# Kernel tuning notes

Hardware: AMD Instinct MI355X
Metric: run time of the kernel (lower is better)

Reference implementation:

```python
import jax, jax.numpy as jnp
import numpy as np

T, DIM, H = 1024, 2048, 16
QLR, KVLR = 1024, 512
NOPE, ROPE, VD = 128, 64, 128
QKD = NOPE + ROPE          # 192
IH, ID, TOPK = 16, 128, 256
EPS = 1e-6

def rmsnorm(x, w):
    return x * jax.lax.rsqrt(jnp.mean(x * x, axis=-1, keepdims=True) + EPS) * w

def layernorm(x, w, b, eps=1e-5):
    m = jnp.mean(x, axis=-1, keepdims=True)
    v = jnp.mean((x - m) ** 2, axis=-1, keepdims=True)
    return (x - m) * jax.lax.rsqrt(v + eps) * w + b

def apply_rope(x, cos, sin):
    # non-interleaved: first half = real, second half = imag
    d = x.shape[-1] // 2
    while cos.ndim < x.ndim:
        cos, sin = cos[:, None], sin[:, None]
    x1, x2 = x[..., :d], x[..., d:]
    return jnp.concatenate([x1 * cos - x2 * sin, x1 * sin + x2 * cos], axis=-1)

def hadamard(x):
    # unnormalized Walsh-Hadamard on last dim (power of 2)
    n = x.shape[-1]
    shape = x.shape
    y, h = x, 1
    while h < n:
        y = y.reshape(shape[:-1] + (-1, 2 * h))
        a, b = y[..., :h], y[..., h:]
        y = jnp.concatenate([a + b, a - b], axis=-1)
        h *= 2
    return y.reshape(shape)

def rotate_activation(x):
    # half-swap then Hadamard on each half
    d = x.shape[-1] // 2
    x1, x2 = x[..., :d], x[..., d:]
    return jnp.concatenate([hadamard(x2), hadamard(x1)], axis=-1)

def setup_inputs() -> dict:
    key = jax.random.key(0)
    ks = jax.random.split(key, 10)
    s = 0.02
    w = lambda k, shp: jax.random.normal(k, shp, jnp.float32) * s
    pos = jnp.arange(T, dtype=jnp.float32)
    inv = 1.0 / (10000.0 ** (jnp.arange(0, ROPE, 2, dtype=jnp.float32) / ROPE))
    ang = pos[:, None] * inv[None, :]
    return {
        'hidden_states': jax.random.normal(ks[0], (T, DIM), jnp.float32),
        'rope_cos': jnp.cos(ang), 'rope_sin': jnp.sin(ang),
        'wq_a': w(ks[1], (QLR, DIM)),
        'q_norm_w': jnp.ones((QLR,), jnp.float32),
        'wq_b': w(ks[2], (H * QKD, QLR)),
        'wkv_a': w(ks[3], (KVLR + ROPE, DIM)),
        'kv_norm_w': jnp.ones((KVLR,), jnp.float32),
        'wkv_b': w(ks[4], (H * (NOPE + VD), KVLR)),
        'wo': w(ks[5], (DIM, H * VD)),
        'iq_norm_w': jnp.ones((QLR,), jnp.float32),
        'iwq_b': w(ks[6], (IH * ID, QLR)),
        'iwk': w(ks[7], (IH * ID, DIM)),
        'k_norm_w': jnp.ones((ID,), jnp.float32),
        'k_norm_b': jnp.zeros((ID,), jnp.float32),
        'wproj': w(ks[8], (IH, DIM)),
    }

def reference(hidden_states, rope_cos, rope_sin, wq_a, q_norm_w, wq_b,
              wkv_a, kv_norm_w, wkv_b, wo, iq_norm_w, iwq_b, iwk,
              k_norm_w, k_norm_b, wproj):
    x = hidden_states
    t = x.shape[0]
    qr = x @ wq_a.T                                   # [t, QLR]

    # ---- lightning indexer: top-k causal token selection ----
    iq = (rmsnorm(qr, iq_norm_w) @ iwq_b.T).reshape(t, IH, ID)
    iq = jnp.concatenate([apply_rope(iq[..., :ROPE], rope_cos, rope_sin), iq[..., ROPE:]], -1)
    iq = rotate_activation(iq)
    ik = layernorm((x @ iwk.T).reshape(t, IH, ID), k_norm_w, k_norm_b)
    ik = jnp.concatenate([apply_rope(ik[..., :ROPE], rope_cos, rope_sin), ik[..., ROPE:]], -1)
    ik = rotate_activation(ik)
    w = (x @ wproj.T) * (IH ** -0.5) * (ID ** -0.5)   # [t, IH]
    dots = jax.nn.relu(jnp.einsum('thd,shd->ths', iq, ik)) * w[:, :, None]
    score = dots.sum(axis=1)                          # [t, t]
    rows = jnp.arange(t)
    score = jnp.where(rows[None, :] <= rows[:, None], score, -jnp.inf)
    _, topk_idx = jax.lax.top_k(score, TOPK)          # [t, TOPK]
    valid = topk_idx <= rows[:, None]
    safe_idx = jnp.where(valid, topk_idx, 0)

    # ---- MLA latent projections ----
    q = (rmsnorm(qr, q_norm_w) @ wq_b.T).reshape(t, H, QKD)
    q_nope, q_pe = q[..., :NOPE], q[..., NOPE:]
    q_pe = apply_rope(q_pe, rope_cos, rope_sin)
    kv_a = x @ wkv_a.T                                # [t, KVLR+ROPE]
    kv = rmsnorm(kv_a[:, :KVLR], kv_norm_w)
    k_pe = apply_rope(kv_a[:, KVLR:], rope_cos, rope_sin)
    wkv = wkv_b.reshape(H, NOPE + VD, KVLR)
    w_k, w_v = wkv[:, :NOPE, :], wkv[:, NOPE:, :]
    q_nope_proj = jnp.einsum('thd,hdc->thc', q_nope, w_k)
    q_key = jnp.concatenate([q_nope_proj, q_pe], -1)  # [t, H, KVLR+ROPE]
    kv_key = jnp.concatenate([kv, k_pe], -1)          # [t, KVLR+ROPE]

    # ---- sparse attention over selected indices ----
    sel = kv_key[safe_idx]                            # [t, TOPK, KVLR+ROPE]
    scale = QKD ** -0.5
    logits = jnp.einsum('thc,tkc->thk', q_key, sel) * scale
    logits = jnp.where(valid[:, None, :], logits, -jnp.inf)
    attn = jax.nn.softmax(logits, axis=-1)
    out_latent = jnp.einsum('thk,tkc->thc', attn, sel[..., :KVLR])
    out_v = jnp.einsum('thc,hdc->thd', out_latent, w_v)
    return out_v.reshape(t, H * VD) @ wo.T            # [t, DIM]
```

## Files before the change

### kernel.cpp

```cpp
#include <hip/hip_runtime.h>
#include <hip/hip_bf16.h>
#include <math.h>

#define T_     1024
#define DIM_   2048
#define H_     16
#define QLR_   1024
#define KVLR_  512
#define NOPE_  128
#define ROPE_  64
#define VD_    128
#define QKD_   192
#define IH_    16
#define ID_    128
#define TOPK_  256
#define CKV_   576

#define SCALE_W    0.022097086912079608f
#define SCALE_LOG  0.07216878364870323f

typedef short bfrag __attribute__((ext_vector_type(8)));
typedef float ffrag __attribute__((ext_vector_type(4)));

__device__ __forceinline__ unsigned short f2bf(float f) {
    union { __hip_bfloat16 h; unsigned short u; } c; c.h = __float2bfloat16(f); return c.u;
}
__device__ __forceinline__ float bf2f(unsigned short u) {
    union { unsigned short u; __hip_bfloat16 h; } c; c.u = u; return __bfloat162float(c.h);
}

__global__ __launch_bounds__(256) void cast_hl_k(
    const float* __restrict__ in, unsigned short* __restrict__ hi,
    unsigned short* __restrict__ lo, long n,
    const float* __restrict__ colw, const float* __restrict__ rowscale, int Kc)
{
    long base = ((long)blockIdx.x * 256 + threadIdx.x) * 4;
    if (base >= n) return;
    float4 v = *(const float4*)(in + base);
    float s[4] = {v.x, v.y, v.z, v.w};
    if (colw) {
        int col = (int)(base % Kc);
        float4 cw = *(const float4*)(colw + col);
        s[0] *= cw.x; s[1] *= cw.y; s[2] *= cw.z; s[3] *= cw.w;
    }
    if (rowscale) {
        float r = rowscale[base / Kc];
        s[0] *= r; s[1] *= r; s[2] *= r; s[3] *= r;
    }
    ushort4 h4;
    h4.x = f2bf(s[0]); h4.y = f2bf(s[1]); h4.z = f2bf(s[2]); h4.w = f2bf(s[3]);
    *(ushort4*)(hi + base) = h4;
    if (lo) {
        ushort4 l4;
        l4.x = f2bf(s[0] - bf2f(h4.x));
        l4.y = f2bf(s[1] - bf2f(h4.y));
        l4.z = f2bf(s[2] - bf2f(h4.z));
        l4.w = f2bf(s[3] - bf2f(h4.w));
        *(ushort4*)(lo + base) = l4;
    }
}

__global__ __launch_bounds__(256) void tcast_k(const float* __restrict__ in,
                                               unsigned short* __restrict__ out)
{
    int h = blockIdx.z, c0 = blockIdx.x * 32, d0 = blockIdx.y * 32;
    __shared__ float t[32][33];
    int tx = threadIdx.x & 31, ty = threadIdx.x >> 5;
    #pragma unroll
    for (int i = 0; i < 4; ++i)
        t[ty + i * 8][tx] = in[(long)(h * 256 + d0 + ty + i * 8) * 512 + c0 + tx];
    __syncthreads();
    #pragma unroll
    for (int i = 0; i < 4; ++i)
        out[((long)h * 512 + c0 + ty + i * 8) * 128 + d0 + tx] = f2bf(t[tx][ty + i * 8]);
}

__global__ __launch_bounds__(256) void gemm_bt_mfma_k(
    const unsigned short* __restrict__ A, const unsigned short* __restrict__ B,
    float* __restrict__ C, long sA, long sB, long sC,
    int lda, int ldb, int ldc, int N, int K)
{
    A += (long)blockIdx.z * sA;
    B += (long)blockIdx.z * sB;
    C += (long)blockIdx.z * sC;
    __shared__ unsigned short As[128 * 40];
    __shared__ unsigned short Bs[128 * 40];
    const int tid = threadIdx.x;
    const int bm = blockIdx.y * 128, bn = blockIdx.x * 128;
    const int wave = tid >> 6, lane = tid & 63;
    const int wm = (wave >> 1) * 64, wn = (wave & 1) * 64;
    const int lm = lane & 15, quad = lane >> 4;

    ffrag acc[4][4];
    #pragma unroll
    for (int mi = 0; mi < 4; ++mi)
        #pragma unroll
        for (int ni = 0; ni < 4; ++ni)
            #pragma unroll
            for (int r = 0; r < 4; ++r) acc[mi][ni][r] = 0.f;

    const int srow = tid >> 1, shalf = tid & 1;
    const long aoff = (long)(bm + srow) * lda + shalf * 16;
    int brow = bn + srow; if (brow > N - 1) brow = N - 1;
    const long boff = (long)brow * ldb + shalf * 16;
    unsigned short* la = As + srow * 40 + shalf * 16;
    unsigned short* lb = Bs + srow * 40 + shalf * 16;

    uint4 va0 = *(const uint4*)(A + aoff);
    uint4 va1 = *(const uint4*)(A + aoff + 8);
    uint4 vb0 = *(const uint4*)(B + boff);
    uint4 vb1 = *(const uint4*)(B + boff + 8);

    for (int k0 = 0; k0 < K; k0 += 32) {
        __syncthreads();
        *(uint4*)la = va0; *(uint4*)(la + 8) = va1;
        *(uint4*)lb = vb0; *(uint4*)(lb + 8) = vb1;
        __syncthreads();
        if (k0 + 32 < K) {
            va0 = *(const uint4*)(A + aoff + k0 + 32);
            va1 = *(const uint4*)(A + aoff + k0 + 40);
            vb0 = *(const uint4*)(B + boff + k0 + 32);
            vb1 = *(const uint4*)(B + boff + k0 + 40);
        }
        bfrag af[4], bf[4];
        #pragma unroll
        for (int mi = 0; mi < 4; ++mi)
            af[mi] = *(const bfrag*)(As + (wm + mi * 16 + lm) * 40 + quad * 8);
        #pragma unroll
        for (int ni = 0; ni < 4; ++ni)
            bf[ni] = *(const bfrag*)(Bs + (wn + ni * 16 + lm) * 40 + quad * 8);
        #pragma unroll
        for (int mi = 0; mi < 4; ++mi)
            #pragma unroll
            for (int ni = 0; ni < 4; ++ni)
                acc[mi][ni] = __builtin_amdgcn_mfma_f32_16x16x32_bf16(
                    af[mi], bf[ni], acc[mi][ni], 0, 0, 0);
    }

    #pragma unroll
    for (int mi = 0; mi < 4; ++mi)
        #pragma unroll
        for (int ni = 0; ni < 4; ++ni) {
            int n = bn + wn + ni * 16 + lm;
            if (n < N) {
                int mb = bm + wm + mi * 16 + quad * 4;
                #pragma unroll
                for (int r = 0; r < 4; ++r)
                    C[(long)(mb + r) * ldc + n] = acc[mi][ni][r];
            }
        }
}

__global__ __launch_bounds__(256) void gemm_bt64_k(
    const unsigned short* __restrict__ A, const unsigned short* __restrict__ B,
    void* __restrict__ Cv, long sA, long sB, long sC,
    int lda, int ldb, int ldc, int N, int K, int obf)
{
    A += (long)blockIdx.z * sA;
    B += (long)blockIdx.z * sB;
    __shared__ unsigned short As[64 * 40];
    __shared__ unsigned short Bs[64 * 40];
    const int tid = threadIdx.x;
    const int bm = blockIdx.y * 64, bn = blockIdx.x * 64;
    const int wave = tid >> 6, lane = tid & 63;
    const int wm = (wave >> 1) * 32, wn = (wave & 1) * 32;
    const int lm = lane & 15, quad = lane >> 4;

    ffrag acc[2][2];
    #pragma unroll
    for (int mi = 0; mi < 2; ++mi)
        #pragma unroll
        for (int ni = 0; ni < 2; ++ni)
            #pragma unroll
            for (int r = 0; r < 4; ++r) acc[mi][ni][r] = 0.f;

    const int srow = tid >> 2, schunk = tid & 3;
    const long aoff = (long)(bm + srow) * lda + schunk * 8;
    int brow = bn + srow; if (brow > N - 1) brow = N - 1;
    const long boff = (long)brow * ldb + schunk * 8;
    unsigned short* la = As + srow * 40 + schunk * 8;
    unsigned short* lb = Bs + srow * 40 + schunk * 8;

    uint4 va = *(const uint4*)(A + aoff);
    uint4 vb = *(const uint4*)(B + boff);

    for (int k0 = 0; k0 < K; k0 += 32) {
        __syncthreads();
        *(uint4*)la = va;
        *(uint4*)lb = vb;
        __syncthreads();
        if (k0 + 32 < K) {
            va = *(const uint4*)(A + aoff + k0 + 32);
            vb = *(const uint4*)(B + boff + k0 + 32);
        }
        bfrag af[2], bf[2];
        #pragma unroll
        for (int mi = 0; mi < 2; ++mi)
            af[mi] = *(const bfrag*)(As + (wm + mi * 16 + lm) * 40 + quad * 8);
        #pragma unroll
        for (int ni = 0; ni < 2; ++ni)
            bf[ni] = *(const bfrag*)(Bs + (wn + ni * 16 + lm) * 40 + quad * 8);
        #pragma unroll
        for (int mi = 0; mi < 2; ++mi)
            #pragma unroll
            for (int ni = 0; ni < 2; ++ni)
                acc[mi][ni] = __builtin_amdgcn_mfma_f32_16x16x32_bf16(
                    af[mi], bf[ni], acc[mi][ni], 0, 0, 0);
    }

    #pragma unroll
    for (int mi = 0; mi < 2; ++mi)
        #pragma unroll
        for (int ni = 0; ni < 2; ++ni) {
            int n = bn + wn + ni * 16 + lm;
            if (n < N) {
                int mb = bm + wm + mi * 16 + quad * 4;
                if (obf) {
                    unsigned short* C = (unsigned short*)Cv + (long)blockIdx.z * sC;
                    #pragma unroll
                    for (int r = 0; r < 4; ++r)
                        C[(long)(mb + r) * ldc + n] = f2bf(acc[mi][ni][r]);
                } else {
                    float* C = (float*)Cv + (long)blockIdx.z * sC;
                    #pragma unroll
                    for (int r = 0; r < 4; ++r)
                        C[(long)(mb + r) * ldc + n] = acc[mi][ni][r];
                }
            }
        }
}

__global__ __launch_bounds__(256) void gemm3_bt64_k(
    const unsigned short* __restrict__ Ah, const unsigned short* __restrict__ Al,
    const unsigned short* __restrict__ Bh, const unsigned short* __restrict__ Bl,
    float* __restrict__ C, int lda, int ldb, int ldc, int K)
{
    __shared__ unsigned short Ahs[64 * 40], Als[64 * 40], Bhs[64 * 40], Bls[64 * 40];
    const int tid = threadIdx.x;
    const int bm = blockIdx.y * 64, bn = blockIdx.x * 64;
    const int wave = tid >> 6, lane = tid & 63;
    const int wm = (wave >> 1) * 32, wn = (wave & 1) * 32;
    const int lm = lane & 15, quad = lane >> 4;

    ffrag acc[2][2];
    #pragma unroll
    for (int mi = 0; mi < 2; ++mi)
        #pragma unroll
        for (int ni = 0; ni < 2; ++ni)
            #pragma unroll
            for (int r = 0; r < 4; ++r) acc[mi][ni][r] = 0.f;

    const int srow = tid >> 2, schunk = tid & 3;
    const long aoff = (long)(bm + srow) * lda + schunk * 8;
    const long boff = (long)(bn + srow) * ldb + schunk * 8;
    const int loff = srow * 40 + schunk * 8;

    uint4 vah = *(const uint4*)(Ah + aoff);
    uint4 val = *(const uint4*)(Al + aoff);
    uint4 vbh = *(const uint4*)(Bh + boff);
    uint4 vbl = *(const uint4*)(Bl + boff);

    for (int k0 = 0; k0 < K; k0 += 32) {
        __syncthreads();
        *(uint4*)(Ahs + loff) = vah;
        *(uint4*)(Als + loff) = val;
        *(uint4*)(Bhs + loff) = vbh;
        *(uint4*)(Bls + loff) = vbl;
        __syncthreads();
        if (k0 + 32 < K) {
            vah = *(const uint4*)(Ah + aoff + k0 + 32);
            val = *(const uint4*)(Al + aoff + k0 + 32);
            vbh = *(const uint4*)(Bh + boff + k0 + 32);
            vbl = *(const uint4*)(Bl + boff + k0 + 32);
        }
        bfrag ah[2], al[2], bh[2], bl[2];
        #pragma unroll
        for (int mi = 0; mi < 2; ++mi) {
            ah[mi] = *(const bfrag*)(Ahs + (wm + mi * 16 + lm) * 40 + quad * 8);
            al[mi] = *(const bfrag*)(Als + (wm + mi * 16 + lm) * 40 + quad * 8);
        }
        #pragma unroll
        for (int ni = 0; ni < 2; ++ni) {
            bh[ni] = *(const bfrag*)(Bhs + (wn + ni * 16 + lm) * 40 + quad * 8);
            bl[ni] = *(const bfrag*)(Bls + (wn + ni * 16 + lm) * 40 + quad * 8);
        }
        #pragma unroll
        for (int mi = 0; mi < 2; ++mi)
            #pragma unroll
            for (int ni = 0; ni < 2; ++ni) {
                acc[mi][ni] = __builtin_amdgcn_mfma_f32_16x16x32_bf16(ah[mi], bh[ni], acc[mi][ni], 0, 0, 0);
                acc[mi][ni] = __builtin_amdgcn_mfma_f32_16x16x32_bf16(ah[mi], bl[ni], acc[mi][ni], 0, 0, 0);
                acc[mi][ni] = __builtin_amdgcn_mfma_f32_16x16x32_bf16(al[mi], bh[ni], acc[mi][ni], 0, 0, 0);
            }
    }

    #pragma unroll
    for (int mi = 0; mi < 2; ++mi)
        #pragma unroll
        for (int ni = 0; ni < 2; ++ni) {
            int n = bn + wn + ni * 16 + lm;
            int mb = bm + wm + mi * 16 + quad * 4;
            #pragma unroll
            for (int r = 0; r < 4; ++r)
                C[(long)(mb + r) * ldc + n] = acc[mi][ni][r];
        }
}

__global__ __launch_bounds__(256) void wtok_k(const float* __restrict__ x,
    const float* __restrict__ wproj, float* __restrict__ wtok)
{
    int t = blockIdx.x, tid = threadIdx.x;
    __shared__ float xs[DIM_];
    for (int c = tid; c < DIM_; c += 256) xs[c] = x[(long)t * DIM_ + c];
    __syncthreads();
    int wave = tid >> 6, lane = tid & 63;
    #pragma unroll
    for (int i = 0; i < 4; ++i) {
        int h = wave * 4 + i;
        float s = 0.f;
        for (int c = lane; c < DIM_; c += 64) s += xs[c] * wproj[(long)h * DIM_ + c];
        for (int off = 32; off; off >>= 1) s += __shfl_xor(s, off, 64);
        if (lane == 0) wtok[(long)t * IH_ + h] = s * SCALE_W;
    }
}

__global__ __launch_bounds__(256) void rstd_k(const float* __restrict__ qr, float* __restrict__ rstd)
{
    int t = blockIdx.x, tid = threadIdx.x;
    float s = 0.f;
    for (int c = tid; c < QLR_; c += 256) { float v = qr[(long)t * QLR_ + c]; s += v * v; }
    __shared__ float red[256];
    red[tid] = s; __syncthreads();
    for (int off = 128; off; off >>= 1) { if (tid < off) red[tid] += red[tid + off]; __syncthreads(); }
    if (tid == 0) rstd[t] = rsqrtf(red[0] / (float)QLR_ + 1e-6f);
}

__device__ __forceinline__ void rope_rotate_128(float* s, float* w2, int tid, int t,
    const float* __restrict__ cosb, const float* __restrict__ sinb)
{
    float n1 = 0.f, n2 = 0.f;
    if (tid < 32) {
        float x1 = s[tid], x2 = s[tid + 32];
        float c = cosb[t * 32 + tid], sn = sinb[t * 32 + tid];
        n1 = x1 * c - x2 * sn;
        n2 = x1 * sn + x2 * c;
    }
    __syncthreads();
    if (tid < 32) { s[tid] = n1; s[tid + 32] = n2; }
    __syncthreads();
    const int g = tid >> 6, p = tid & 63;
    w2[tid] = s[((1 - g) << 6) + p];
    __syncthreads();
    #pragma unroll
    for (int h = 1; h < 64; h <<= 1) {
        float a = w2[tid], b = w2[(g << 6) + (p ^ h)];
        __syncthreads();
        w2[tid] = (p & h) ? (b - a) : (a + b);
        __syncthreads();
    }
}

__global__ __launch_bounds__(128) void transform_iq_k(float* __restrict__ iq,
    const float* __restrict__ cosb, const float* __restrict__ sinb)
{
    int row = blockIdx.x;
    int t = row / IH_;
    int tid = threadIdx.x;
    __shared__ float s[128], w2[128];
    s[tid] = iq[(long)row * 128 + tid];
    __syncthreads();
    rope_rotate_128(s, w2, tid, t, cosb, sinb);
    iq[(long)row * 128 + tid] = w2[tid];
}

__global__ __launch_bounds__(128) void transform_ik_k(float* __restrict__ ik,
    const float* __restrict__ knw, const float* __restrict__ knb,
    const float* __restrict__ cosb, const float* __restrict__ sinb)
{
    int row = blockIdx.x;
    int t = row / IH_;
    int tid = threadIdx.x;
    __shared__ float s[128], w2[128], red[128];
    float v = ik[(long)row * 128 + tid];
    red[tid] = v; __syncthreads();
    for (int off = 64; off; off >>= 1) { if (tid < off) red[tid] += red[tid + off]; __syncthreads(); }
    float m = red[0] / 128.f; __syncthreads();
    float d = v - m;
    red[tid] = d * d; __syncthreads();
    for (int off = 64; off; off >>= 1) { if (tid < off) red[tid] += red[tid + off]; __syncthreads(); }
    float var = red[0] / 128.f;
    s[tid] = d * rsqrtf(var + 1e-5f) * knw[tid] + knb[tid];
    __syncthreads();
    rope_rotate_128(s, w2, tid, t, cosb, sinb);
    ik[(long)row * 128 + tid] = w2[tid];
}

__global__ __launch_bounds__(256) void transform_kv_k(const float* __restrict__ kva,
    float* __restrict__ kvkey, const float* __restrict__ kvnw,
    const float* __restrict__ cosb, const float* __restrict__ sinb)
{
    int t = blockIdx.x, tid = threadIdx.x;
    const float* a = kva + (long)t * CKV_;
    float* o = kvkey + (long)t * CKV_;
    float v0 = a[tid], v1 = a[tid + 256];
    __shared__ float red[256];
    __shared__ float rsh;
    red[tid] = v0 * v0 + v1 * v1; __syncthreads();
    for (int off = 128; off; off >>= 1) { if (tid < off) red[tid] += red[tid + off]; __syncthreads(); }
    if (tid == 0) rsh = rsqrtf(red[0] / (float)KVLR_ + 1e-6f);
    __syncthreads();
    float rs = rsh;
    o[tid]       = v0 * rs * kvnw[tid];
    o[tid + 256] = v1 * rs * kvnw[tid + 256];
    if (tid < 32) {
        float x1 = a[512 + tid], x2 = a[544 + tid];
        float c = cosb[t * 32 + tid], sn = sinb[t * 32 + tid];
        o[512 + tid] = x1 * c - x2 * sn;
        o[544 + tid] = x1 * sn + x2 * c;
    }
}

__global__ __launch_bounds__(64) void qpe_k(const float* __restrict__ q, float* __restrict__ qkey,
    const float* __restrict__ cosb, const float* __restrict__ sinb)
{
    int row = blockIdx.x * 2 + (threadIdx.x >> 5);
    int i = threadIdx.x & 31;
    int t = row / H_;
    const float* qp = q + (long)row * QKD_ + NOPE_;
    float x1 = qp[i], x2 = qp[i + 32];
    float c = cosb[t * 32 + i], sn = sinb[t * 32 + i];
    float* o = qkey + (long)row * CKV_ + 512;
    o[i]      = x1 * c - x2 * sn;
    o[i + 32] = x1 * sn + x2 * c;
}

__global__ __launch_bounds__(256) void score3_k(
    const unsigned short* __restrict__ iqh, const unsigned short* __restrict__ iql,
    const unsigned short* __restrict__ ikh, const unsigned short* __restrict__ ikl,
    const float* __restrict__ wtok, float* __restrict__ score)
{
    const int bt = blockIdx.y, bs = blockIdx.x;
    if (bs > bt) return;
    __shared__ unsigned short Ah[64 * 40], Al[64 * 40], Bh[64 * 40], Bl[64 * 40];
    __shared__ float wts[64][16];
    const int tid = threadIdx.x;
    const int wave = tid >> 6, lane = tid & 63;
    const int wm = (wave >> 1) * 32, wn = (wave & 1) * 32;
    const int lm = lane & 15, quad = lane >> 4;
    const int t0 = bt * 64, s0 = bs * 64;
    const int srow = tid >> 2, schunk = tid & 3;
    const int loff = srow * 40 + schunk * 8;

    for (int e = tid; e < 1024; e += 256)
        wts[e >> 4][e & 15] = wtok[(long)(t0 + (e >> 4)) * IH_ + (e & 15)];

    const long abase = (long)(t0 + srow) * 2048 + schunk * 8;
    const long bbase = (long)(s0 + srow) * 2048 + schunk * 8;

    uint4 pah = *(const uint4*)(iqh + abase);
    uint4 pal = *(const uint4*)(iql + abase);
    uint4 pbh = *(const uint4*)(ikh + bbase);
    uint4 pbl = *(const uint4*)(ikl + bbase);

    float accf[2][2][4] = {};

    for (int h = 0; h < IH_; ++h) {
        ffrag acch[2][2];
        #pragma unroll
        for (int mi = 0; mi < 2; ++mi)
            #pragma unroll
            for (int ni = 0; ni < 2; ++ni)
                #pragma unroll
                for (int r = 0; r < 4; ++r) acch[mi][ni][r] = 0.f;

        #pragma unroll
        for (int k0 = 0; k0 < ID_; k0 += 32) {
            __syncthreads();
            *(uint4*)(Ah + loff) = pah;
            *(uint4*)(Al + loff) = pal;
            *(uint4*)(Bh + loff) = pbh;
            *(uint4*)(Bl + loff) = pbl;
            __syncthreads();
            int step = h * 4 + (k0 >> 5) + 1;
            if (step < 64) {
                int off = (step >> 2) * 128 + (step & 3) * 32;
                pah = *(const uint4*)(iqh + abase + off);
                pal = *(const uint4*)(iql + abase + off);
                pbh = *(const uint4*)(ikh + bbase + off);
                pbl = *(const uint4*)(ikl + bbase + off);
            }
            bfrag ahf[2], alf[2], bhf[2], blf[2];
            #pragma unroll
            for (int mi = 0; mi < 2; ++mi) {
                ahf[mi] = *(const bfrag*)(Ah + (wm + mi * 16 + lm) * 40 + quad * 8);
                alf[mi] = *(const bfrag*)(Al + (wm + mi * 16 + lm) * 40 + quad * 8);
            }
            #pragma unroll
            for (int ni = 0; ni < 2; ++ni) {
                bhf[ni] = *(const bfrag*)(Bh + (wn + ni * 16 + lm) * 40 + quad * 8);
                blf[ni] = *(const bfrag*)(Bl + (wn + ni * 16 + lm) * 40 + quad * 8);
            }
            #pragma unroll
            for (int mi = 0; mi < 2; ++mi)
                #pragma unroll
                for (int ni = 0; ni < 2; ++ni) {
                    acch[mi][ni] = __builtin_amdgcn_mfma_f32_16x16x32_bf16(ahf[mi], bhf[ni], acch[mi][ni], 0, 0, 0);
                    acch[mi][ni] = __builtin_amdgcn_mfma_f32_16x16x32_bf16(ahf[mi], blf[ni], acch[mi][ni], 0, 0, 0);
                    acch[mi][ni] = __builtin_amdgcn_mfma_f32_16x16x32_bf16(alf[mi], bhf[ni], acch[mi][ni], 0, 0, 0);
                }
        }
        #pragma unroll
        for (int mi = 0; mi < 2; ++mi) {
            float wr[4];
            #pragma unroll
            for (int r = 0; r < 4; ++r) wr[r] = wts[wm + mi * 16 + quad * 4 + r][h];
            #pragma unroll
            for (int ni = 0; ni < 2; ++ni)
                #pragma unroll
                for (int r = 0; r < 4; ++r)
                    accf[mi][ni][r] += fmaxf(acch[mi][ni][r], 0.f) * wr[r];
        }
    }
    #pragma unroll
    for (int mi = 0; mi < 2; ++mi)
        #pragma unroll
        for (int ni = 0; ni < 2; ++ni) {
            int s = s0 + wn + ni * 16 + lm;
            int tb = t0 + wm + mi * 16 + quad * 4;
            #pragma unroll
            for (int r = 0; r < 4; ++r)
                score[(long)(tb + r) * T_ + s] = accf[mi][ni][r];
        }
}

__global__ __launch_bounds__(512) void topk_k(const float* __restrict__ score, int* __restrict__ topk)
{
    int t = blockIdx.x, tid = threadIdx.x;
    __shared__ float v[1024];
    __shared__ int ix[1024];
    for (int i = tid; i < 1024; i += 512) {
        v[i] = (i <= t) ? score[(long)t * T_ + i] : -INFINITY;
        ix[i] = i;
    }
    __syncthreads();
    for (int k = 2; k <= 1024; k <<= 1) {
        for (int j = k >> 1; j > 0; j >>= 1) {
            for (int i = tid; i < 1024; i += 512) {
                int l = i ^ j;
                if (l > i) {
                    bool up = ((i & k) == 0);
                    float vi = v[i], vl = v[l];
                    int xi = ix[i], xl = ix[l];
                    bool iBetter = (vi > vl) || (vi == vl && xi < xl);
                    bool doSwap = up ? !iBetter : iBetter;
                    if (doSwap) { v[i] = vl; v[l] = vi; ix[i] = xl; ix[l] = xi; }
                }
            }
            __syncthreads();
        }
    }
    if (tid < 256) topk[(long)t * TOPK_ + tid] = ix[tid];
}

__global__ __launch_bounds__(256) void attn3_k(
    const float* __restrict__ qkey, const unsigned short* __restrict__ kvb,
    const int* __restrict__ topkp, unsigned short* __restrict__ olat)
{
    __shared__ unsigned short U[23808];
    __shared__ float red[16 * 17];
    __shared__ int kidx[256];
    unsigned short* Qbf  = U;
    unsigned short* SelA = U + 9344;
    float*          Lg   = (float*)(U + 9344);
    unsigned short* Pbf  = U + 19584;
    unsigned short* VT   = U;

    const int t = blockIdx.x, tid = threadIdx.x;
    const int wave = tid >> 6, lane = tid & 63;
    const int lm = lane & 15, quad = lane >> 4;

    kidx[tid] = topkp[(long)t * TOPK_ + tid];
    const float4* q4 = (const float4*)(qkey + (long)t * (H_ * CKV_));
    #pragma unroll
    for (int rep = 0; rep < 9; ++rep) {
        int e4 = rep * 256 + tid;
        float4 v = q4[e4];
        int f = e4 * 4, h = f / CKV_, c = f - h * CKV_;
        ushort4 u4; u4.x = f2bf(v.x); u4.y = f2bf(v.y); u4.z = f2bf(v.z); u4.w = f2bf(v.w);
        *(ushort4*)(Qbf + h * 584 + c) = u4;
    }
    __syncthreads();

    const int ukey = tid >> 2, uoff = (tid & 3) * 8;
    int myk[4];
    #pragma unroll
    for (int rep = 0; rep < 4; ++rep) myk[rep] = kidx[rep * 64 + ukey];

    ffrag acc[4];
    #pragma unroll
    for (int ni = 0; ni < 4; ++ni)
        #pragma unroll
        for (int r = 0; r < 4; ++r) acc[ni][r] = 0.f;

    for (int c0 = 0; c0 < CKV_; c0 += 32) {
        __syncthreads();
        #pragma unroll
        for (int rep = 0; rep < 4; ++rep) {
            uint4 v = *(const uint4*)(kvb + (long)myk[rep] * CKV_ + c0 + uoff);
            *(uint4*)(SelA + (rep * 64 + ukey) * 40 + uoff) = v;
        }
        __syncthreads();
        bfrag af = *(const bfrag*)(Qbf + lm * 584 + c0 + quad * 8);
        #pragma unroll
        for (int ni = 0; ni < 4; ++ni) {
            bfrag bf = *(const bfrag*)(SelA + (wave * 64 + ni * 16 + lm) * 40 + quad * 8);
            acc[ni] = __builtin_amdgcn_mfma_f32_16x16x32_bf16(af, bf, acc[ni], 0, 0, 0);
        }
    }
    __syncthreads();
    #pragma unroll
    for (int ni = 0; ni < 4; ++ni)
        #pragma unroll
        for (int r = 0; r < 4; ++r)
            Lg[(quad * 4 + r) * 260 + wave * 64 + ni * 16 + lm] = acc[ni][r];
    __syncthreads();

    {
        int h = tid >> 4, j = tid & 15;
        float m = -INFINITY;
        #pragma unroll
        for (int kk = 0; kk < 16; ++kk) {
            int key = j * 16 + kk;
            if (kidx[key] <= t) m = fmaxf(m, Lg[h * 260 + key]);
        }
        red[h * 17 + j] = m;
        __syncthreads();
        float mh = -INFINITY;
        #pragma unroll
        for (int jj = 0; jj < 16; ++jj) mh = fmaxf(mh, red[h * 17 + jj]);
        __syncthreads();
        float s = 0.f;
        float pv[16];
        #pragma unroll
        for (int kk = 0; kk < 16; ++kk) {
            int key = j * 16 + kk;
            float e = (kidx[key] <= t) ? expf(Lg[h * 260 + key] * SCALE_LOG - mh * SCALE_LOG) : 0.f;
            pv[kk] = e; s += e;
        }
        red[h * 17 + j] = s;
        __syncthreads();
        float sh = 0.f;
        #pragma unroll
        for (int jj = 0; jj < 16; ++jj) sh += red[h * 17 + jj];
        float inv = 1.f / sh;
        #pragma unroll
        for (int kk = 0; kk < 16; ++kk)
            Pbf[h * 264 + j * 16 + kk] = f2bf(pv[kk] * inv);
    }
    __syncthreads();

    const int kp = tid & 15, cg = tid >> 4;
    ffrag acc2[8];
    #pragma unroll
    for (int ci = 0; ci < 8; ++ci)
        #pragma unroll
        for (int r = 0; r < 4; ++r) acc2[ci][r] = 0.f;

    for (int k0 = 0; k0 < TOPK_; k0 += 32) {
        __syncthreads();
        {
            int ka = kidx[k0 + 2 * kp], kb = kidx[k0 + 2 * kp + 1];
            const unsigned short* ra = kvb + (long)ka * CKV_ + cg * 32;
            const unsigned short* rb = kvb + (long)kb * CKV_ + cg * 32;
            #pragma unroll
            for (int half = 0; half < 2; ++half) {
                uint4 a0 = *(const uint4*)(ra + half * 16);
                uint4 a1 = *(const uint4*)(ra + half * 16 + 8);
                uint4 b0 = *(const uint4*)(rb + half * 16);
                uint4 b1 = *(const uint4*)(rb + half * 16 + 8);
                const unsigned short* pa_ = (const unsigned short*)&a0;
                const unsigned short* pb_ = (const unsigned short*)&b0;
                #pragma unroll
                for (int i = 0; i < 8; ++i) {
                    int c = cg * 32 + half * 16 + i;
                    *(unsigned int*)(VT + c * 36 + 2 * kp) =
                        (unsigned int)pa_[i] | ((unsigned int)pb_[i] << 16);
                }
                pa_ = (const unsigned short*)&a1;
                pb_ = (const unsigned short*)&b1;
                #pragma unroll
                for (int i = 0; i < 8; ++i) {
                    int c = cg * 32 + half * 16 + 8 + i;
                    *(unsigned int*)(VT + c * 36 + 2 * kp) =
                        (unsigned int)pa_[i] | ((unsigned int)pb_[i] << 16);
                }
            }
        }
        __syncthreads();
        bfrag pa = *(const bfrag*)(Pbf + lm * 264 + k0 + quad * 8);
        #pragma unroll
        for (int ci = 0; ci < 8; ++ci) {
            int c = wave * 128 + ci * 16 + lm;
            bfrag bv;
            ((uint2*)&bv)[0] = *(const uint2*)(VT + c * 36 + quad * 8);
            ((uint2*)&bv)[1] = *(const uint2*)(VT + c * 36 + quad * 8 + 4);
            acc2[ci] = __builtin_amdgcn_mfma_f32_16x16x32_bf16(pa, bv, acc2[ci], 0, 0, 0);
        }
    }
    #pragma unroll
    for (int ci = 0; ci < 8; ++ci)
        #pragma unroll
        for (int r = 0; r < 4; ++r)
            olat[((long)t * H_ + quad * 4 + r) * 512 + wave * 128 + ci * 16 + lm] = f2bf(acc2[ci][r]);
}

extern "C" void kernel_launch(void* const* d_in, const int* in_sizes, int n_in,
                              void* d_out, int out_size, void* d_ws, size_t ws_size,
                              hipStream_t stream)
{
    const float* x          = (const float*)d_in[0];
    const float* cosb       = (const float*)d_in[1];
    const float* sinb       = (const float*)d_in[2];
    const float* wq_a       = (const float*)d_in[3];
    const float* q_norm_w   = (const float*)d_in[4];
    const float* wq_b       = (const float*)d_in[5];
    const float* wkv_a      = (const float*)d_in[6];
    const float* kv_norm_w  = (const float*)d_in[7];
    const float* wkv_b      = (const float*)d_in[8];
    const float* wo         = (const float*)d_in[9];
    const float* iq_norm_w  = (const float*)d_in[10];
    const float* iwq_b      = (const float*)d_in[11];
    const float* iwk        = (const float*)d_in[12];
    const float* k_norm_w   = (const float*)d_in[13];
    const float* k_norm_b   = (const float*)d_in[14];
    const float* wproj      = (const float*)d_in[15];
    float* out = (float*)d_out;

    float* ws    = (float*)d_ws;
    float* qr    = ws;
    float* rstd  = ws + 1048576;
    float* wtok  = ws + 1049600;
    float* kvkey = ws + 1065984;
    int*   topk  = (int*)(ws + 1655808);
    float* qkey  = ws + 1917952;
    float* outv  = ws + 11355136;
    float* U0    = ws + 13452288;
    float* iq    = U0;
    float* ik    = U0 + 2097152;
    float* kva   = U0 + 4194304;
    float* qbuf  = U0 + 4784128;
    float* score = U0 + 7929856;

    unsigned short* qkey_u = (unsigned short*)qkey;
    unsigned short* wqa_hi  = qkey_u;
    unsigned short* wqa_lo  = qkey_u + 2097152;
    unsigned short* iwk_hi  = qkey_u + 4194304;
    unsigned short* iwk_lo  = qkey_u + 8388608;
    unsigned short* iwqb_hi = qkey_u + 12582912;
    unsigned short* iwqb_lo = qkey_u + 14680064;
    unsigned short* qriq_hi = qkey_u + 16777216;
    unsigned short* qriq_lo = qkey_u + 17825792;
    unsigned short* iqbf_hi = qkey_u;
    unsigned short* iqbf_lo = qkey_u + 2097152;
    unsigned short* ikbf_hi = qkey_u + 4194304;
    unsigned short* ikbf_lo = qkey_u + 6291456;
    unsigned short* wkvb_bf = qkey_u + 8388608;
    unsigned short* wo_bf   = qkey_u + 12582912;
    unsigned short* q_u     = (unsigned short*)qbuf;
    unsigned short* x_hi    = q_u;
    unsigned short* x_lo    = q_u + 2097152;
    unsigned short* wkva_hi = q_u + 4194304;
    unsigned short* outv_u  = (unsigned short*)outv;
    unsigned short* wqb_hi  = outv_u;
    unsigned short* qrq_hi  = outv_u + 3145728;
    unsigned short* outv_bf = outv_u;
    unsigned short* qbf     = (unsigned short*)iq;
    unsigned short* wkT     = (unsigned short*)ik;
    unsigned short* kvb     = (unsigned short*)qr;
    unsigned short* olat_bf = (unsigned short*)U0;

    #define CAST(src, hi, lo, n, cw, rs, K) \
        cast_hl_k<<<(n)/1024, 256, 0, stream>>>((src), (hi), (lo), (n), (cw), (rs), (K))

    CAST(x,     x_hi,   x_lo,   2097152L, nullptr, nullptr, 0);
    CAST(wq_a,  wqa_hi, wqa_lo, 2097152L, nullptr, nullptr, 0);
    CAST(iwk,   iwk_hi, iwk_lo, 4194304L, nullptr, nullptr, 0);
    CAST(iwq_b, iwqb_hi,iwqb_lo,2097152L, nullptr, nullptr, 0);
    CAST(wkv_a, wkva_hi,nullptr,1179648L, nullptr, nullptr, 0);
    CAST(wq_b,  wqb_hi, nullptr,3145728L, nullptr, nullptr, 0);

    gemm3_bt64_k<<<dim3(QLR_/64, T_/64), 256, 0, stream>>>(
        x_hi, x_lo, wqa_hi, wqa_lo, qr, DIM_, DIM_, QLR_, DIM_);

    rstd_k<<<T_, 256, 0, stream>>>(qr, rstd);
    CAST(qr, qriq_hi, qriq_lo, 1048576L, iq_norm_w, rstd, QLR_);
    CAST(qr, qrq_hi,  nullptr, 1048576L, q_norm_w,  rstd, QLR_);

    gemm3_bt64_k<<<dim3(IH_*ID_/64, T_/64), 256, 0, stream>>>(
        qriq_hi, qriq_lo, iwqb_hi, iwqb_lo, iq, QLR_, QLR_, IH_*ID_, QLR_);
    gemm3_bt64_k<<<dim3(IH_*ID_/64, T_/64), 256, 0, stream>>>(
        x_hi, x_lo, iwk_hi, iwk_lo, ik, DIM_, DIM_, IH_*ID_, DIM_);

    gemm_bt64_k<<<dim3((CKV_+63)/64, T_/64, 1), 256, 0, stream>>>(
        x_hi, wkva_hi, kva, 0,0,0, DIM_, DIM_, CKV_, CKV_, DIM_, 0);

    gemm_bt64_k<<<dim3(H_*QKD_/64, T_/64, 1), 256, 0, stream>>>(
        qrq_hi, wqb_hi, qbuf, 0,0,0, QLR_, QLR_, H_*QKD_, H_*QKD_, QLR_, 0);

    wtok_k<<<T_, 256, 0, stream>>>(x, wproj, wtok);

    transform_iq_k<<<T_*IH_, 128, 0, stream>>>(iq, cosb, sinb);
    transform_ik_k<<<T_*IH_, 128, 0, stream>>>(ik, k_norm_w, k_norm_b, cosb, sinb);
    transform_kv_k<<<T_, 256, 0, stream>>>(kva, kvkey, kv_norm_w, cosb, sinb);

    CAST(kvkey, kvb, nullptr, 589824L, nullptr, nullptr, 0);

    CAST(iq, iqbf_hi, iqbf_lo, 2097152L, nullptr, nullptr, 0);
    CAST(ik, ikbf_hi, ikbf_lo, 2097152L, nullptr, nullptr, 0);
    score3_k<<<dim3(T_/64, T_/64), 256, 0, stream>>>(iqbf_hi, iqbf_lo, ikbf_hi, ikbf_lo, wtok, score);
    topk_k<<<T_, 512, 0, stream>>>(score, topk);

    CAST(qbuf, qbf, nullptr, 3145728L, nullptr, nullptr, 0);
    tcast_k<<<dim3(16, 4, 16), 256, 0, stream>>>(wkv_b, wkT);
    qpe_k<<<T_*H_/2, 64, 0, stream>>>(qbuf, qkey, cosb, sinb);
    gemm_bt_mfma_k<<<dim3(KVLR_/128, T_/128, H_), 256, 0, stream>>>(
        qbf, wkT, qkey, 192L, 65536L, 576L, H_*QKD_, ID_, H_*CKV_, KVLR_, ID_);

    attn3_k<<<T_, 256, 0, stream>>>(qkey, kvb, topk, olat_bf);

    CAST(wkv_b, wkvb_bf, nullptr, 2097152L, nullptr, nullptr, 0);
    gemm_bt64_k<<<dim3(VD_/64, T_/64, H_), 256, 0, stream>>>(
        olat_bf, wkvb_bf + (long)NOPE_*KVLR_, outv_bf,
        512L, (long)(NOPE_+VD_)*KVLR_, (long)VD_,
        H_*KVLR_, KVLR_, H_*VD_, VD_, KVLR_, 1);

    CAST(wo, wo_bf, nullptr, 4194304L, nullptr, nullptr, 0);
    gemm_bt64_k<<<dim3(DIM_/64, T_/64, 1), 256, 0, stream>>>(
        outv_bf, wo_bf, out, 0,0,0, H_*VD_, H_*VD_, DIM_, DIM_, H_*VD_, 0);

    #undef CAST
    (void)in_sizes; (void)n_in; (void)out_size; (void)ws_size;
}
```

Measured before the change: 592.1 us.

## Stream attention keys from global into MFMA fragments and halve LDS footprint

The QK stage now loads each wave's key fragments directly from global memory into registers, with a one-step register prefetch, instead of staging selected keys through LDS with two barriers per chunk. The PV stage processes the 512 latent columns in two passes of 256 to halve the transposed-V LDS tile, and prefetches the next chunk's global loads while the MFMAs run. Together these cut shared memory from about 48KB to about 28KB and set launch bounds to 4 blocks per CU to raise occupancy. In exchange each wave issues more uncoalesced global loads of key rows, gathered keys are fetched twice in PV, and register pressure rises from the prefetch buffers.

```diff
diff --git a/kernel.cpp b/kernel.cpp
--- a/kernel.cpp
+++ b/kernel.cpp
@@ -562,18 +562,17 @@
     if (tid < 256) topk[(long)t * TOPK_ + tid] = ix[tid];
 }
 
-__global__ __launch_bounds__(256) void attn3_k(
+__global__ __launch_bounds__(256, 4) void attn3_k(
     const float* __restrict__ qkey, const unsigned short* __restrict__ kvb,
     const int* __restrict__ topkp, unsigned short* __restrict__ olat)
 {
-    __shared__ unsigned short U[23808];
+    __shared__ unsigned short U[13568];
     __shared__ float red[16 * 17];
     __shared__ int kidx[256];
-    unsigned short* Qbf  = U;
-    unsigned short* SelA = U + 9344;
-    float*          Lg   = (float*)(U + 9344);
-    unsigned short* Pbf  = U + 19584;
-    unsigned short* VT   = U;
+    unsigned short* Qbf = U;
+    float*          Lg  = (float*)U;
+    unsigned short* VT  = U;
+    unsigned short* Pbf = U + 9344;
 
     const int t = blockIdx.x, tid = threadIdx.x;
     const int wave = tid >> 6, lane = tid & 63;
@@ -589,12 +588,11 @@
         ushort4 u4; u4.x = f2bf(v.x); u4.y = f2bf(v.y); u4.z = f2bf(v.z); u4.w = f2bf(v.w);
         *(ushort4*)(Qbf + h * 584 + c) = u4;
     }
-    __syncthreads();
-
-    const int ukey = tid >> 2, uoff = (tid & 3) * 8;
     int myk[4];
     #pragma unroll
-    for (int rep = 0; rep < 4; ++rep) myk[rep] = kidx[rep * 64 + ukey];
+    for (int ni = 0; ni < 4; ++ni)
+        myk[ni] = topkp[(long)t * TOPK_ + wave * 64 + ni * 16 + lm];
+    __syncthreads();
 
     ffrag acc[4];
     #pragma unroll
@@ -602,21 +600,35 @@
         #pragma unroll
         for (int r = 0; r < 4; ++r) acc[ni][r] = 0.f;
 
+    const unsigned short* kb0 = kvb + (long)myk[0] * CKV_ + quad * 8;
+    const unsigned short* kb1 = kvb + (long)myk[1] * CKV_ + quad * 8;
+    const unsigned short* kb2 = kvb + (long)myk[2] * CKV_ + quad * 8;
+    const unsigned short* kb3 = kvb + (long)myk[3] * CKV_ + quad * 8;
+
+    bfrag bcur[4], bnext[4];
+    bcur[0] = *(const bfrag*)(kb0);
+    bcur[1] = *(const bfrag*)(kb1);
+    bcur[2] = *(const bfrag*)(kb2);
+    bcur[3] = *(const bfrag*)(kb3);
+
     for (int c0 = 0; c0 < CKV_; c0 += 32) {
-        __syncthreads();
-        #pragma unroll
-        for (int rep = 0; rep < 4; ++rep) {
-            uint4 v = *(const uint4*)(kvb + (long)myk[rep] * CKV_ + c0 + uoff);
-            *(uint4*)(SelA + (rep * 64 + ukey) * 40 + uoff) = v;
-        }
-        __syncthreads();
+        if (c0 + 32 < CKV_) {
+            bnext[0] = *(const bfrag*)(kb0 + c0 + 32);
+            bnext[1] = *(const bfrag*)(kb1 + c0 + 32);
+            bnext[2] = *(const bfrag*)(kb2 + c0 + 32);
+            bnext[3] = *(const bfrag*)(kb3 + c0 + 32);
+        } else {
+            #pragma unroll
+            for (int ni = 0; ni < 4; ++ni) bnext[ni] = bcur[ni];
+        }
         bfrag af = *(const bfrag*)(Qbf + lm * 584 + c0 + quad * 8);
         #pragma unroll
-        for (int ni = 0; ni < 4; ++ni) {
-            bfrag bf = *(const bfrag*)(SelA + (wave * 64 + ni * 16 + lm) * 40 + quad * 8);
-            acc[ni] = __builtin_amdgcn_mfma_f32_16x16x32_bf16(af, bf, acc[ni], 0, 0, 0);
-        }
-    }
+        for (int ni = 0; ni < 4; ++ni)
+            acc[ni] = __builtin_amdgcn_mfma_f32_16x16x32_bf16(af, bcur[ni], acc[ni], 0, 0, 0);
+        #pragma unroll
+        for (int ni = 0; ni < 4; ++ni) bcur[ni] = bnext[ni];
+    }
+
     __syncthreads();
     #pragma unroll
     for (int ni = 0; ni < 4; ++ni)
@@ -657,61 +669,67 @@
         for (int kk = 0; kk < 16; ++kk)
             Pbf[h * 264 + j * 16 + kk] = f2bf(pv[kk] * inv);
     }
-    __syncthreads();
 
     const int kp = tid & 15, cg = tid >> 4;
-    ffrag acc2[8];
-    #pragma unroll
-    for (int ci = 0; ci < 8; ++ci)
+    ffrag acc2[4];
+    #pragma unroll
+    for (int ci = 0; ci < 4; ++ci)
         #pragma unroll
         for (int r = 0; r < 4; ++r) acc2[ci][r] = 0.f;
 
-    for (int k0 = 0; k0 < TOPK_; k0 += 32) {
+    uint4 a0, a1, b0, b1;
+    #define PREF(IT) { \
+        int p_ = (IT) >> 3, k0p_ = ((IT) & 7) * 32; \
+        int ka_ = kidx[k0p_ + 2 * kp], kb_ = kidx[k0p_ + 2 * kp + 1]; \
+        const unsigned short* ra_ = kvb + (long)ka_ * CKV_ + p_ * 256 + cg * 16; \
+        const unsigned short* rb_ = kvb + (long)kb_ * CKV_ + p_ * 256 + cg * 16; \
+        a0 = *(const uint4*)(ra_);     a1 = *(const uint4*)(ra_ + 8); \
+        b0 = *(const uint4*)(rb_);     b1 = *(const uint4*)(rb_ + 8); }
+
+    PREF(0);
+    for (int it = 0; it < 16; ++it) {
         __syncthreads();
         {
-            int ka = kidx[k0 + 2 * kp], kb = kidx[k0 + 2 * kp + 1];
-            const unsigned short* ra = kvb + (long)ka * CKV_ + cg * 32;
-            const unsigned short* rb = kvb + (long)kb * CKV_ + cg * 32;
-            #pragma unroll
-            for (int half = 0; half < 2; ++half) {
-                uint4 a0 = *(const uint4*)(ra + half * 16);
-                uint4 a1 = *(const uint4*)(ra + half * 16 + 8);
-                uint4 b0 = *(const uint4*)(rb + half * 16);
-                uint4 b1 = *(const uint4*)(rb + half * 16 + 8);
-                const unsigned short* pa_ = (const unsigned short*)&a0;
-                const unsigned short* pb_ = (const unsigned short*)&b0;
-                #pragma unroll
-                for (int i = 0; i < 8; ++i) {
-                    int c = cg * 32 + half * 16 + i;
-                    *(unsigned int*)(VT + c * 36 + 2 * kp) =
-                        (unsigned int)pa_[i] | ((unsigned int)pb_[i] << 16);
-                }
-                pa_ = (const unsigned short*)&a1;
-                pb_ = (const unsigned short*)&b1;
-                #pragma unroll
-                for (int i = 0; i < 8; ++i) {
-                    int c = cg * 32 + half * 16 + 8 + i;
-                    *(unsigned int*)(VT + c * 36 + 2 * kp) =
-                        (unsigned int)pa_[i] | ((unsigned int)pb_[i] << 16);
-                }
-            }
-        }
-        __syncthreads();
+            const unsigned short* pa_ = (const unsigned short*)&a0;
+            const unsigned short* pb_ = (const unsigned short*)&b0;
+            #pragma unroll
+            for (int i = 0; i < 8; ++i)
+                *(unsigned int*)(VT + (cg * 16 + i) * 36 + 2 * kp) =
+                    (unsigned int)pa_[i] | ((unsigned int)pb_[i] << 16);
+            pa_ = (const unsigned short*)&a1;
+            pb_ = (const unsigned short*)&b1;
+            #pragma unroll
+            for (int i = 0; i < 8; ++i)
+                *(unsigned int*)(VT + (cg * 16 + 8 + i) * 36 + 2 * kp) =
+                    (unsigned int)pa_[i] | ((unsigned int)pb_[i] << 16);
+        }
+        __syncthreads();
+        if (it + 1 < 16) PREF(it + 1);
+        int k0 = (it & 7) * 32;
         bfrag pa = *(const bfrag*)(Pbf + lm * 264 + k0 + quad * 8);
         #pragma unroll
-        for (int ci = 0; ci < 8; ++ci) {
-            int c = wave * 128 + ci * 16 + lm;
+        for (int ci = 0; ci < 4; ++ci) {
+            int c = wave * 64 + ci * 16 + lm;
             bfrag bv;
             ((uint2*)&bv)[0] = *(const uint2*)(VT + c * 36 + quad * 8);
             ((uint2*)&bv)[1] = *(const uint2*)(VT + c * 36 + quad * 8 + 4);
             acc2[ci] = __builtin_amdgcn_mfma_f32_16x16x32_bf16(pa, bv, acc2[ci], 0, 0, 0);
         }
-    }
-    #pragma unroll
-    for (int ci = 0; ci < 8; ++ci)
-        #pragma unroll
-        for (int r = 0; r < 4; ++r)
-            olat[((long)t * H_ + quad * 4 + r) * 512 + wave * 128 + ci * 16 + lm] = f2bf(acc2[ci][r]);
+        if ((it & 7) == 7) {
+            int p = it >> 3;
+            #pragma unroll
+            for (int ci = 0; ci < 4; ++ci)
+                #pragma unroll
+                for (int r = 0; r < 4; ++r)
+                    olat[((long)t * H_ + quad * 4 + r) * 512 + p * 256 + wave * 64 + ci * 16 + lm]
+                        = f2bf(acc2[ci][r]);
+            #pragma unroll
+            for (int ci = 0; ci < 4; ++ci)
+                #pragma unroll
+                for (int r = 0; r < 4; ++r) acc2[ci][r] = 0.f;
+        }
+    }
+    #undef PREF
 }
 
 extern "C" void kernel_launch(void* const* d_in, const int* in_sizes, int n_in,
```

After: 601.2 us. No clear change (+1.5%).

## Register-prefetch attention gathers and double-buffer transposed V tiles in LDS

Applied to the files above, without the earlier changes.

Phase A now has each lane gather its key rows straight from global memory into registers, using a three-deep rotating prefetch, instead of staging selected keys through shared memory behind two barriers per step. Phase B splits the 512 latent columns into four passes with smaller per-wave accumulators. It double-buffers the transposed V tiles in LDS, prefetching the next gather into registers while MFMAs run on the current buffer. Shared memory is shrunk and launch bounds request 4 blocks per CU to raise occupancy. The cost is more redundant global loads of key rows (each key row is read by 16 lanes across quads), and a hand-written lgkmcnt wait plus raw barrier that synchronise only LDS traffic.

```diff
diff --git a/kernel.cpp b/kernel.cpp
--- a/kernel.cpp
+++ b/kernel.cpp
@@ -562,18 +562,18 @@
     if (tid < 256) topk[(long)t * TOPK_ + tid] = ix[tid];
 }
 
-__global__ __launch_bounds__(256) void attn3_k(
+__global__ __launch_bounds__(256, 4) void attn3_k(
     const float* __restrict__ qkey, const unsigned short* __restrict__ kvb,
     const int* __restrict__ topkp, unsigned short* __restrict__ olat)
 {
-    __shared__ unsigned short U[23808];
+    __shared__ unsigned short U[13568];
     __shared__ float red[16 * 17];
     __shared__ int kidx[256];
-    unsigned short* Qbf  = U;
-    unsigned short* SelA = U + 9344;
-    float*          Lg   = (float*)(U + 9344);
-    unsigned short* Pbf  = U + 19584;
-    unsigned short* VT   = U;
+    unsigned short* Qbf = U;
+    float*          Lg  = (float*)U;
+    unsigned short* VT0 = U;
+    unsigned short* VT1 = U + 4608;
+    unsigned short* Pbf = U + 9344;
 
     const int t = blockIdx.x, tid = threadIdx.x;
     const int wave = tid >> 6, lane = tid & 63;
@@ -589,12 +589,11 @@
         ushort4 u4; u4.x = f2bf(v.x); u4.y = f2bf(v.y); u4.z = f2bf(v.z); u4.w = f2bf(v.w);
         *(ushort4*)(Qbf + h * 584 + c) = u4;
     }
-    __syncthreads();
-
-    const int ukey = tid >> 2, uoff = (tid & 3) * 8;
-    int myk[4];
-    #pragma unroll
-    for (int rep = 0; rep < 4; ++rep) myk[rep] = kidx[rep * 64 + ukey];
+    int myk0 = topkp[(long)t * TOPK_ + wave * 64 + 0 * 16 + lm];
+    int myk1 = topkp[(long)t * TOPK_ + wave * 64 + 1 * 16 + lm];
+    int myk2 = topkp[(long)t * TOPK_ + wave * 64 + 2 * 16 + lm];
+    int myk3 = topkp[(long)t * TOPK_ + wave * 64 + 3 * 16 + lm];
+    __syncthreads();
 
     ffrag acc[4];
     #pragma unroll
@@ -602,21 +601,34 @@
         #pragma unroll
         for (int r = 0; r < 4; ++r) acc[ni][r] = 0.f;
 
-    for (int c0 = 0; c0 < CKV_; c0 += 32) {
-        __syncthreads();
-        #pragma unroll
-        for (int rep = 0; rep < 4; ++rep) {
-            uint4 v = *(const uint4*)(kvb + (long)myk[rep] * CKV_ + c0 + uoff);
-            *(uint4*)(SelA + (rep * 64 + ukey) * 40 + uoff) = v;
-        }
-        __syncthreads();
-        bfrag af = *(const bfrag*)(Qbf + lm * 584 + c0 + quad * 8);
-        #pragma unroll
-        for (int ni = 0; ni < 4; ++ni) {
-            bfrag bf = *(const bfrag*)(SelA + (wave * 64 + ni * 16 + lm) * 40 + quad * 8);
-            acc[ni] = __builtin_amdgcn_mfma_f32_16x16x32_bf16(af, bf, acc[ni], 0, 0, 0);
-        }
-    }
+    const unsigned short* kb0 = kvb + (long)myk0 * CKV_ + quad * 8;
+    const unsigned short* kb1 = kvb + (long)myk1 * CKV_ + quad * 8;
+    const unsigned short* kb2 = kvb + (long)myk2 * CKV_ + quad * 8;
+    const unsigned short* kb3 = kvb + (long)myk3 * CKV_ + quad * 8;
+
+    bfrag ba[4], bb[4], bc[4];
+    #define LDT(DST, C) { \
+        DST[0] = *(const bfrag*)(kb0 + (C)); \
+        DST[1] = *(const bfrag*)(kb1 + (C)); \
+        DST[2] = *(const bfrag*)(kb2 + (C)); \
+        DST[3] = *(const bfrag*)(kb3 + (C)); }
+    #define PHA_STEP(I, BUF) { \
+        bfrag af = *(const bfrag*)(Qbf + lm * 584 + (I) * 32 + quad * 8); \
+        _Pragma("unroll") \
+        for (int ni = 0; ni < 4; ++ni) \
+            acc[ni] = __builtin_amdgcn_mfma_f32_16x16x32_bf16(af, BUF[ni], acc[ni], 0, 0, 0); \
+        if ((I) < 15) LDT(BUF, (I) * 32 + 96) }
+
+    LDT(ba, 0) LDT(bb, 32) LDT(bc, 64)
+    PHA_STEP(0, ba)  PHA_STEP(1, bb)  PHA_STEP(2, bc)
+    PHA_STEP(3, ba)  PHA_STEP(4, bb)  PHA_STEP(5, bc)
+    PHA_STEP(6, ba)  PHA_STEP(7, bb)  PHA_STEP(8, bc)
+    PHA_STEP(9, ba)  PHA_STEP(10, bb) PHA_STEP(11, bc)
+    PHA_STEP(12, ba) PHA_STEP(13, bb) PHA_STEP(14, bc)
+    PHA_STEP(15, ba) PHA_STEP(16, bb) PHA_STEP(17, bc)
+    #undef PHA_STEP
+    #undef LDT
+
     __syncthreads();
     #pragma unroll
     for (int ni = 0; ni < 4; ++ni)
@@ -657,61 +669,73 @@
         for (int kk = 0; kk < 16; ++kk)
             Pbf[h * 264 + j * 16 + kk] = f2bf(pv[kk] * inv);
     }
-    __syncthreads();
-
-    const int kp = tid & 15, cg = tid >> 4;
-    ffrag acc2[8];
-    #pragma unroll
-    for (int ci = 0; ci < 8; ++ci)
+
+    const int kpair = tid & 15, cgrp = tid >> 4;
+    ffrag acc2[2];
+    #pragma unroll
+    for (int ci = 0; ci < 2; ++ci)
         #pragma unroll
         for (int r = 0; r < 4; ++r) acc2[ci][r] = 0.f;
 
-    for (int k0 = 0; k0 < TOPK_; k0 += 32) {
-        __syncthreads();
-        {
-            int ka = kidx[k0 + 2 * kp], kb = kidx[k0 + 2 * kp + 1];
-            const unsigned short* ra = kvb + (long)ka * CKV_ + cg * 32;
-            const unsigned short* rb = kvb + (long)kb * CKV_ + cg * 32;
-            #pragma unroll
-            for (int half = 0; half < 2; ++half) {
-                uint4 a0 = *(const uint4*)(ra + half * 16);
-                uint4 a1 = *(const uint4*)(ra + half * 16 + 8);
-                uint4 b0 = *(const uint4*)(rb + half * 16);
-                uint4 b1 = *(const uint4*)(rb + half * 16 + 8);
-                const unsigned short* pa_ = (const unsigned short*)&a0;
-                const unsigned short* pb_ = (const unsigned short*)&b0;
-                #pragma unroll
-                for (int i = 0; i < 8; ++i) {
-                    int c = cg * 32 + half * 16 + i;
-                    *(unsigned int*)(VT + c * 36 + 2 * kp) =
-                        (unsigned int)pa_[i] | ((unsigned int)pb_[i] << 16);
-                }
-                pa_ = (const unsigned short*)&a1;
-                pb_ = (const unsigned short*)&b1;
-                #pragma unroll
-                for (int i = 0; i < 8; ++i) {
-                    int c = cg * 32 + half * 16 + 8 + i;
-                    *(unsigned int*)(VT + c * 36 + 2 * kp) =
-                        (unsigned int)pa_[i] | ((unsigned int)pb_[i] << 16);
-                }
-            }
-        }
-        __syncthreads();
-        bfrag pa = *(const bfrag*)(Pbf + lm * 264 + k0 + quad * 8);
-        #pragma unroll
-        for (int ci = 0; ci < 8; ++ci) {
-            int c = wave * 128 + ci * 16 + lm;
-            bfrag bv;
-            ((uint2*)&bv)[0] = *(const uint2*)(VT + c * 36 + quad * 8);
-            ((uint2*)&bv)[1] = *(const uint2*)(VT + c * 36 + quad * 8 + 4);
-            acc2[ci] = __builtin_amdgcn_mfma_f32_16x16x32_bf16(pa, bv, acc2[ci], 0, 0, 0);
-        }
-    }
-    #pragma unroll
-    for (int ci = 0; ci < 8; ++ci)
-        #pragma unroll
-        for (int r = 0; r < 4; ++r)
-            olat[((long)t * H_ + quad * 4 + r) * 512 + wave * 128 + ci * 16 + lm] = f2bf(acc2[ci][r]);
+    uint4 ga0, gb0, ga1, gb1;
+    #define PREFB(GA, GB, IT) { \
+        int ka_ = kidx[((IT) & 7) * 32 + 2 * kpair]; \
+        int kb_ = kidx[((IT) & 7) * 32 + 2 * kpair + 1]; \
+        long co_ = (long)(((IT) >> 3) * 128 + cgrp * 8); \
+        GA = *(const uint4*)(kvb + (long)ka_ * CKV_ + co_); \
+        GB = *(const uint4*)(kvb + (long)kb_ * CKV_ + co_); }
+    #define STOREB(GA, GB, BUF) { \
+        const unsigned short* pa_ = (const unsigned short*)&GA; \
+        const unsigned short* pb_ = (const unsigned short*)&GB; \
+        _Pragma("unroll") \
+        for (int i_ = 0; i_ < 8; ++i_) \
+            *(unsigned int*)((BUF) + (cgrp * 8 + i_) * 36 + 2 * kpair) = \
+                (unsigned int)pa_[i_] | ((unsigned int)pb_[i_] << 16); }
+    #define MFMAB(BUF, IT) { \
+        bfrag pa = *(const bfrag*)(Pbf + lm * 264 + ((IT) & 7) * 32 + quad * 8); \
+        _Pragma("unroll") \
+        for (int ci = 0; ci < 2; ++ci) { \
+            int c = wave * 32 + ci * 16 + lm; \
+            bfrag bv; \
+            ((uint2*)&bv)[0] = *(const uint2*)((BUF) + c * 36 + quad * 8); \
+            ((uint2*)&bv)[1] = *(const uint2*)((BUF) + c * 36 + quad * 8 + 4); \
+            acc2[ci] = __builtin_amdgcn_mfma_f32_16x16x32_bf16(pa, bv, acc2[ci], 0, 0, 0); } }
+    #define OLATST(IT) { \
+        int p_ = (IT) >> 3; \
+        _Pragma("unroll") \
+        for (int ci = 0; ci < 2; ++ci) \
+            _Pragma("unroll") \
+            for (int r = 0; r < 4; ++r) \
+                olat[((long)t * H_ + quad * 4 + r) * 512 + p_ * 128 + wave * 32 + ci * 16 + lm] \
+                    = f2bf(acc2[ci][r]); \
+        _Pragma("unroll") \
+        for (int ci = 0; ci < 2; ++ci) \
+            _Pragma("unroll") \
+            for (int r = 0; r < 4; ++r) acc2[ci][r] = 0.f; }
+    #define LGKBAR() { asm volatile("s_waitcnt lgkmcnt(0)" ::: "memory"); \
+                       __builtin_amdgcn_s_barrier(); }
+
+    PREFB(ga0, gb0, 0);
+    PREFB(ga1, gb1, 1);
+    LGKBAR();
+    STOREB(ga0, gb0, VT0);
+    LGKBAR();
+    for (int it = 0; it < 32; it += 2) {
+        STOREB(ga1, gb1, VT1);
+        MFMAB(VT0, it);
+        if (it + 2 < 32) PREFB(ga0, gb0, it + 2);
+        LGKBAR();
+        if (it + 2 < 32) STOREB(ga0, gb0, VT0);
+        MFMAB(VT1, it + 1);
+        if (it + 3 < 32) PREFB(ga1, gb1, it + 3);
+        if (((it + 1) & 7) == 7) OLATST(it + 1);
+        LGKBAR();
+    }
+    #undef PREFB
+    #undef STOREB
+    #undef MFMAB
+    #undef OLATST
+    #undef LGKBAR
 }
 
 extern "C" void kernel_launch(void* const* d_in, const int* in_sizes, int n_in,
```

New measurement: 596.0 us. About the same (+0.7%).
